# Optimization experiments

Hardware: AMD Instinct MI355X
Metric: run time of the kernel (lower is better)

The kernel has to match this reference:

```python
import jax, jax.numpy as jnp
import numpy as np

NEG = -9e15

def setup_inputs() -> dict:
    key = jax.random.key(0)
    k1, k2, k3, k4 = jax.random.split(key, 4)
    N, Fin, Fout = 8192, 256, 256
    h = jax.random.normal(k1, (N, Fin), dtype=jnp.float32)
    adj = jax.random.randint(k2, (N, N), 0, 2).astype(jnp.float32)
    W = jax.random.normal(k3, (Fin, Fout), dtype=jnp.float32) * (1.414 * np.sqrt(2.0 / (Fin + Fout)))
    a = jax.random.normal(k4, (2 * Fout, 1), dtype=jnp.float32) * (1.414 * np.sqrt(2.0 / (2 * Fout + 1)))
    return {"h": h, "adj": adj, "W": W, "a": a}

def reference(h, adj, W, a):
    Fout = W.shape[1]
    Wh = h @ W                                  # [N, Fout]
    Wh1 = Wh @ a[:Fout, :]                      # [N, 1]
    Wh2 = Wh @ a[Fout:, :]                      # [N, 1]
    e = jax.nn.leaky_relu(Wh1 + Wh2.T, 0.2)     # [N, N]
    mask = (adj > 0).astype(e.dtype)
    e = e * mask + NEG * (1.0 - mask)
    attention = jax.nn.softmax(e, axis=1)       # [N, N]
    h_prime = attention @ Wh                    # [N, Fout]
    return jax.nn.elu(h_prime)
```

## Files before the change

### kernel.cpp

```cpp
#include <hip/hip_runtime.h>
#include <hip/hip_bf16.h>
#include <stdint.h>

typedef __attribute__((ext_vector_type(4))) short short4v;
typedef __attribute__((ext_vector_type(8))) short short8v;
typedef __attribute__((ext_vector_type(4))) float float4v;

#define NN 8192
#define FIN 256
#define FOUT 256

__device__ __forceinline__ short f2bf(float f) {
    unsigned u = __float_as_uint(f);
    unsigned r = u + 0x7fffu + ((u >> 16) & 1u);
    return (short)(r >> 16);
}

__global__ __launch_bounds__(256) void k_wt(const float* __restrict__ W, short* __restrict__ WT) {
    int k = blockIdx.x, n = threadIdx.x;
    WT[n * 256 + k] = f2bf(W[k * 256 + n]);
}

__global__ __launch_bounds__(256) void k_gemm1(const float* __restrict__ h, const short* __restrict__ WT,
                                               float* __restrict__ Wh) {
    __shared__ short sA[64 * 40];
    __shared__ short sB[64 * 40];
    int bm = blockIdx.x;
    int bn = blockIdx.y;
    int t  = threadIdx.x;
    int w = t >> 6, lane = t & 63, quad = lane >> 4, l16 = lane & 15;

    float4v acc[4];
#pragma unroll
    for (int c = 0; c < 4; c++)
#pragma unroll
        for (int j = 0; j < 4; j++) acc[c][j] = 0.f;

    int r  = t >> 2;
    int ko = (t & 3) * 8;

    for (int k0 = 0; k0 < 256; k0 += 32) {
        const float4v* src = (const float4v*)&h[(size_t)(64 * bm + r) * 256 + k0 + ko];
        float4v v0 = src[0], v1 = src[1];
        short8v pk;
        pk[0] = f2bf(v0[0]); pk[1] = f2bf(v0[1]); pk[2] = f2bf(v0[2]); pk[3] = f2bf(v0[3]);
        pk[4] = f2bf(v1[0]); pk[5] = f2bf(v1[1]); pk[6] = f2bf(v1[2]); pk[7] = f2bf(v1[3]);
        *(short8v*)&sA[r * 40 + ko] = pk;
        short8v bv = *(const short8v*)&WT[(size_t)(64 * bn + r) * 256 + k0 + ko];
        *(short8v*)&sB[r * 40 + ko] = bv;
        __syncthreads();

        short8v af = *(const short8v*)&sA[(16 * w + l16) * 40 + quad * 8];
#pragma unroll
        for (int c = 0; c < 4; c++) {
            short8v bf = *(const short8v*)&sB[(16 * c + l16) * 40 + quad * 8];
            acc[c] = __builtin_amdgcn_mfma_f32_16x16x32_bf16(af, bf, acc[c], 0, 0, 0);
        }
        __syncthreads();
    }
#pragma unroll
    for (int c = 0; c < 4; c++)
#pragma unroll
        for (int j = 0; j < 4; j++) {
            int row = 64 * bm + 16 * w + quad * 4 + j;
            int col = 64 * bn + 16 * c + l16;
            Wh[(size_t)row * 256 + col] = acc[c][j];
        }
}

__global__ __launch_bounds__(256) void k_rowstats(const float* __restrict__ Wh, const float* __restrict__ a,
                                                  float* __restrict__ Wh1, float* __restrict__ Wh2,
                                                  unsigned* __restrict__ maxenc) {
    int w = threadIdx.x >> 6, lane = threadIdx.x & 63;
    int row = blockIdx.x * 4 + w;
    float s1 = 0.f, s2 = 0.f;
#pragma unroll
    for (int j = 0; j < 4; j++) {
        int c = lane + 64 * j;
        float v = Wh[(size_t)row * 256 + c];
        s1 += v * a[c];
        s2 += v * a[256 + c];
    }
#pragma unroll
    for (int off = 32; off; off >>= 1) {
        s1 += __shfl_down(s1, off);
        s2 += __shfl_down(s2, off);
    }
    if (lane == 0) {
        Wh1[row] = s1;
        Wh2[row] = s2;
        unsigned u = __float_as_uint(s2);
        unsigned key = (u & 0x80000000u) ? ~u : (u | 0x80000000u);
        atomicMax(maxenc, key);
    }
}

__global__ __launch_bounds__(256) void k_transpose(const float* __restrict__ Wh, short* __restrict__ WhT) {
    __shared__ short sT[64 * 72];
    int bm = blockIdx.x, bn = blockIdx.y;
    int t = threadIdx.x;
#pragma unroll
    for (int i = 0; i < 4; i++) {
        int idx = i * 256 + t;
        int r = idx >> 4, c4 = (idx & 15) * 4;
        float4v v = *(const float4v*)&Wh[(size_t)(64 * bm + r) * 256 + 64 * bn + c4];
#pragma unroll
        for (int j = 0; j < 4; j++) sT[(c4 + j) * 72 + r] = f2bf(v[j]);
    }
    __syncthreads();
    int c = t >> 2, ro = (t & 3) * 16;
#pragma unroll
    for (int hh = 0; hh < 2; hh++) {
        short8v v = *(const short8v*)&sT[c * 72 + ro + 8 * hh];
        *(short8v*)&WhT[(size_t)(64 * bn + c) * 8192 + 64 * bm + ro + 8 * hh] = v;
    }
}

__global__ __launch_bounds__(1024, 4) void k_gat(const float* __restrict__ adj, const short* __restrict__ WhT,
                                                 const float* __restrict__ Wh1, const float* __restrict__ Wh2,
                                                 const unsigned* __restrict__ maxenc,
                                                 float* __restrict__ Cacc, float* __restrict__ Lacc,
                                                 int Ksub) {
    __shared__ short sB[256 * 64];
    __shared__ short sA[64 * 72];
    int bm = blockIdx.x;
    int sidx = blockIdx.y;
    int kb = sidx * Ksub;
    int t = threadIdx.x;
    int lane = t & 63, quad = lane >> 4, l16 = lane & 15;
    int w = t >> 6;
    int rg = w & 3;
    int cg = w >> 2;

    unsigned key = maxenc[0];
    unsigned u = (key & 0x80000000u) ? (key & 0x7fffffffu) : ~key;
    float maxw2 = __uint_as_float(u);

    int r  = t >> 4;
    int kc = (t & 15) * 4;
    float wh1r = Wh1[64 * bm + r];
    float sup = wh1r + maxw2;
    float ci = fmaxf(sup, 0.2f * sup);

    const float* adj_row = &adj[(size_t)(64 * bm + r) * 8192 + kb];
    const float* w2base  = &Wh2[kb];

    int schunk = (t & 7) ^ ((t >> 3) & 7);
    const short* gb0 = &WhT[(size_t)(t >> 3) * 8192 + kb + schunk * 8];
    short* lb0 = &sB[(w * 64 + lane) * 8];

    float4v acc[4];
#pragma unroll
    for (int c = 0; c < 4; c++)
#pragma unroll
        for (int j = 0; j < 4; j++) acc[c][j] = 0.f;
    float lsum = 0.f;

    float4v av = *(const float4v*)&adj_row[kc];
    float4v w2 = *(const float4v*)&w2base[kc];

    for (int k0 = 0; k0 < Ksub; k0 += 64) {
#pragma unroll
        for (int i = 0; i < 2; i++) {
            __builtin_amdgcn_global_load_lds(
                (const __attribute__((address_space(1))) void*)(gb0 + (size_t)i * 128 * 8192 + k0),
                (__attribute__((address_space(3))) void*)(lb0 + i * 1024 * 8),
                16, 0, 0);
        }
        short4v pk;
#pragma unroll
        for (int j = 0; j < 4; j++) {
            float s = wh1r + w2[j];
            float f = fmaxf(s, 0.2f * s);
            float p = __expf(f - ci);
            p = (av[j] > 0.f) ? p : 0.f;
            lsum += p;
            pk[j] = f2bf(p);
        }
        *(short4v*)&sA[r * 72 + kc] = pk;
        if (k0 + 64 < Ksub) {
            av = *(const float4v*)&adj_row[k0 + 64 + kc];
            w2 = *(const float4v*)&w2base[k0 + 64 + kc];
        }
        __syncthreads();

#pragma unroll
        for (int kk = 0; kk < 2; kk++) {
            short8v af = *(const short8v*)&sA[(16 * rg + l16) * 72 + kk * 32 + quad * 8];
#pragma unroll
            for (int c = 0; c < 4; c++) {
                int n = 64 * cg + 16 * c + l16;
                int ch = (kk * 4 + quad) ^ (n & 7);
                short8v bf = *(const short8v*)&sB[n * 64 + ch * 8];
                acc[c] = __builtin_amdgcn_mfma_f32_16x16x32_bf16(af, bf, acc[c], 0, 0, 0);
            }
        }
        __syncthreads();
    }

#pragma unroll
    for (int off = 8; off; off >>= 1) lsum += __shfl_xor(lsum, off, 16);
    if ((lane & 15) == 0) atomicAdd(&Lacc[64 * bm + r], lsum);

#pragma unroll
    for (int c = 0; c < 4; c++)
#pragma unroll
        for (int j = 0; j < 4; j++) {
            int rl = 16 * rg + quad * 4 + j;
            int row = 64 * bm + rl;
            int col = 64 * cg + 16 * c + l16;
            atomicAdd(&Cacc[(size_t)row * 256 + col], acc[c][j]);
        }
}

__global__ __launch_bounds__(256) void k_final(const float* __restrict__ Cacc, const float* __restrict__ Lacc,
                                               float* __restrict__ out) {
    int idx = blockIdx.x * 256 + threadIdx.x;
    int row = idx >> 6;
    int c4 = (idx & 63) * 4;
    float4v v = *(const float4v*)&Cacc[(size_t)row * 256 + c4];
    float inv = 1.0f / fmaxf(Lacc[row], 1e-30f);
    float4v o;
#pragma unroll
    for (int j = 0; j < 4; j++) {
        float x = v[j] * inv;
        o[j] = (x > 0.f) ? x : (__expf(x) - 1.f);
    }
    *(float4v*)&out[(size_t)row * 256 + c4] = o;
}

extern "C" void kernel_launch(void* const* d_in, const int* in_sizes, int n_in,
                              void* d_out, int out_size, void* d_ws, size_t ws_size,
                              hipStream_t stream) {
    const float* h   = (const float*)d_in[0];
    const float* adj = (const float*)d_in[1];
    const float* W   = (const float*)d_in[2];
    const float* a   = (const float*)d_in[3];
    float* out = (float*)d_out;

    const int S = 4;
    const int Ksub = NN / S;

    char* ws = (char*)d_ws;
    float*    Wh     = (float*)(ws);
    float*    Cacc   = (float*)(ws);
    short*    WhT    = (short*)(ws + 8388608);
    char*     tail   = ws + 12582912;
    short*    WT     = (short*)(tail);
    float*    Wh1    = (float*)(tail + 131072);
    float*    Wh2    = (float*)(tail + 163840);
    float*    Lacc   = (float*)(tail + 196608);
    unsigned* maxenc = (unsigned*)(tail + 229376);

    hipMemsetAsync(maxenc, 0, sizeof(unsigned), stream);

    k_wt<<<256, 256, 0, stream>>>(W, WT);
    k_gemm1<<<dim3(128, 4), 256, 0, stream>>>(h, WT, Wh);
    k_rowstats<<<2048, 256, 0, stream>>>(Wh, a, Wh1, Wh2, maxenc);
    k_transpose<<<dim3(128, 4), 256, 0, stream>>>(Wh, WhT);
    hipMemsetAsync(Cacc, 0, (size_t)NN * 256 * sizeof(float), stream);
    hipMemsetAsync(Lacc, 0, (size_t)NN * sizeof(float), stream);
    k_gat<<<dim3(128, S), 1024, 0, stream>>>(adj, WhT, Wh1, Wh2, maxenc, Cacc, Lacc, Ksub);
    k_final<<<2048, 256, 0, stream>>>(Cacc, Lacc, out);
}
```

Measured before the change: 539.9 us.

## Halve k_gat block to 512 threads with 32x64 warp tiles

```diff
diff --git a/kernel.cpp b/kernel.cpp
--- a/kernel.cpp
+++ b/kernel.cpp
@@ -116,11 +116,11 @@
     }
 }
 
-__global__ __launch_bounds__(1024, 4) void k_gat(const float* __restrict__ adj, const short* __restrict__ WhT,
-                                                 const float* __restrict__ Wh1, const float* __restrict__ Wh2,
-                                                 const unsigned* __restrict__ maxenc,
-                                                 float* __restrict__ Cacc, float* __restrict__ Lacc,
-                                                 int Ksub) {
+__global__ __launch_bounds__(512, 4) void k_gat(const float* __restrict__ adj, const short* __restrict__ WhT,
+                                                const float* __restrict__ Wh1, const float* __restrict__ Wh2,
+                                                const unsigned* __restrict__ maxenc,
+                                                float* __restrict__ Cacc, float* __restrict__ Lacc,
+                                                int Ksub) {
     __shared__ short sB[256 * 64];
     __shared__ short sA[64 * 72];
     int bm = blockIdx.x;
@@ -129,15 +129,15 @@
     int t = threadIdx.x;
     int lane = t & 63, quad = lane >> 4, l16 = lane & 15;
     int w = t >> 6;
-    int rg = w & 3;
-    int cg = w >> 2;
+    int mr = (w >> 2) * 32;
+    int cg = w & 3;
 
     unsigned key = maxenc[0];
     unsigned u = (key & 0x80000000u) ? (key & 0x7fffffffu) : ~key;
     float maxw2 = __uint_as_float(u);
 
-    int r  = t >> 4;
-    int kc = (t & 15) * 4;
+    int r  = t >> 3;
+    int kc = (t & 7) * 8;
     float wh1r = Wh1[64 * bm + r];
     float sup = wh1r + maxw2;
     float ci = fmaxf(sup, 0.2f * sup);
@@ -147,70 +147,88 @@
 
     int schunk = (t & 7) ^ ((t >> 3) & 7);
     const short* gb0 = &WhT[(size_t)(t >> 3) * 8192 + kb + schunk * 8];
-    short* lb0 = &sB[(w * 64 + lane) * 8];
-
-    float4v acc[4];
-#pragma unroll
-    for (int c = 0; c < 4; c++)
-#pragma unroll
-        for (int j = 0; j < 4; j++) acc[c][j] = 0.f;
+    short* lb0 = &sB[t * 8];
+
+    float4v acc[2][4];
+#pragma unroll
+    for (int rt = 0; rt < 2; rt++)
+#pragma unroll
+        for (int c = 0; c < 4; c++)
+#pragma unroll
+            for (int j = 0; j < 4; j++) acc[rt][c][j] = 0.f;
     float lsum = 0.f;
 
-    float4v av = *(const float4v*)&adj_row[kc];
-    float4v w2 = *(const float4v*)&w2base[kc];
+    float4v av0 = *(const float4v*)&adj_row[kc];
+    float4v av1 = *(const float4v*)&adj_row[kc + 4];
+    float4v w20 = *(const float4v*)&w2base[kc];
+    float4v w21 = *(const float4v*)&w2base[kc + 4];
 
     for (int k0 = 0; k0 < Ksub; k0 += 64) {
 #pragma unroll
-        for (int i = 0; i < 2; i++) {
+        for (int i = 0; i < 4; i++) {
             __builtin_amdgcn_global_load_lds(
-                (const __attribute__((address_space(1))) void*)(gb0 + (size_t)i * 128 * 8192 + k0),
-                (__attribute__((address_space(3))) void*)(lb0 + i * 1024 * 8),
+                (const __attribute__((address_space(1))) void*)(gb0 + (size_t)i * 64 * 8192 + k0),
+                (__attribute__((address_space(3))) void*)(lb0 + i * 512 * 8),
                 16, 0, 0);
         }
-        short4v pk;
+        short8v pk;
 #pragma unroll
         for (int j = 0; j < 4; j++) {
-            float s = wh1r + w2[j];
+            float s = wh1r + w20[j];
             float f = fmaxf(s, 0.2f * s);
             float p = __expf(f - ci);
-            p = (av[j] > 0.f) ? p : 0.f;
+            p = (av0[j] > 0.f) ? p : 0.f;
             lsum += p;
             pk[j] = f2bf(p);
         }
-        *(short4v*)&sA[r * 72 + kc] = pk;
+#pragma unroll
+        for (int j = 0; j < 4; j++) {
+            float s = wh1r + w21[j];
+            float f = fmaxf(s, 0.2f * s);
+            float p = __expf(f - ci);
+            p = (av1[j] > 0.f) ? p : 0.f;
+            lsum += p;
+            pk[4 + j] = f2bf(p);
+        }
+        *(short8v*)&sA[r * 72 + kc] = pk;
         if (k0 + 64 < Ksub) {
-            av = *(const float4v*)&adj_row[k0 + 64 + kc];
-            w2 = *(const float4v*)&w2base[k0 + 64 + kc];
+            av0 = *(const float4v*)&adj_row[k0 + 64 + kc];
+            av1 = *(const float4v*)&adj_row[k0 + 64 + kc + 4];
+            w20 = *(const float4v*)&w2base[k0 + 64 + kc];
+            w21 = *(const float4v*)&w2base[k0 + 64 + kc + 4];
         }
         __syncthreads();
 
 #pragma unroll
         for (int kk = 0; kk < 2; kk++) {
-            short8v af = *(const short8v*)&sA[(16 * rg + l16) * 72 + kk * 32 + quad * 8];
+            short8v af0 = *(const short8v*)&sA[(mr + l16) * 72 + kk * 32 + quad * 8];
+            short8v af1 = *(const short8v*)&sA[(mr + 16 + l16) * 72 + kk * 32 + quad * 8];
 #pragma unroll
             for (int c = 0; c < 4; c++) {
                 int n = 64 * cg + 16 * c + l16;
                 int ch = (kk * 4 + quad) ^ (n & 7);
                 short8v bf = *(const short8v*)&sB[n * 64 + ch * 8];
-                acc[c] = __builtin_amdgcn_mfma_f32_16x16x32_bf16(af, bf, acc[c], 0, 0, 0);
+                acc[0][c] = __builtin_amdgcn_mfma_f32_16x16x32_bf16(af0, bf, acc[0][c], 0, 0, 0);
+                acc[1][c] = __builtin_amdgcn_mfma_f32_16x16x32_bf16(af1, bf, acc[1][c], 0, 0, 0);
             }
         }
         __syncthreads();
     }
 
 #pragma unroll
-    for (int off = 8; off; off >>= 1) lsum += __shfl_xor(lsum, off, 16);
-    if ((lane & 15) == 0) atomicAdd(&Lacc[64 * bm + r], lsum);
-
-#pragma unroll
-    for (int c = 0; c < 4; c++)
-#pragma unroll
-        for (int j = 0; j < 4; j++) {
-            int rl = 16 * rg + quad * 4 + j;
-            int row = 64 * bm + rl;
-            int col = 64 * cg + 16 * c + l16;
-            atomicAdd(&Cacc[(size_t)row * 256 + col], acc[c][j]);
-        }
+    for (int off = 4; off; off >>= 1) lsum += __shfl_xor(lsum, off, 8);
+    if ((t & 7) == 0) atomicAdd(&Lacc[64 * bm + r], lsum);
+
+#pragma unroll
+    for (int rt = 0; rt < 2; rt++)
+#pragma unroll
+        for (int c = 0; c < 4; c++)
+#pragma unroll
+            for (int j = 0; j < 4; j++) {
+                int row = 64 * bm + mr + rt * 16 + quad * 4 + j;
+                int col = 64 * cg + 16 * c + l16;
+                atomicAdd(&Cacc[(size_t)row * 256 + col], acc[rt][c][j]);
+            }
 }
 
 __global__ __launch_bounds__(256) void k_final(const float* __restrict__ Cacc, const float* __restrict__ Lacc,
@@ -260,6 +278,6 @@
     k_transpose<<<dim3(128, 4), 256, 0, stream>>>(Wh, WhT);
     hipMemsetAsync(Cacc, 0, (size_t)NN * 256 * sizeof(float), stream);
     hipMemsetAsync(Lacc, 0, (size_t)NN * sizeof(float), stream);
-    k_gat<<<dim3(128, S), 1024, 0, stream>>>(adj, WhT, Wh1, Wh2, maxenc, Cacc, Lacc, Ksub);
+    k_gat<<<dim3(128, S), 512, 0, stream>>>(adj, WhT, Wh1, Wh2, maxenc, Cacc, Lacc, Ksub);
     k_final<<<2048, 256, 0, stream>>>(Cacc, Lacc, out);
 }
```

After: 542.8 us. No clear change (+0.5%).

## Register-prefetch WhT tiles and software-pipeline the GAT attention loop

Applied to the files above, without the earlier changes.

```diff
diff --git a/kernel.cpp b/kernel.cpp
--- a/kernel.cpp
+++ b/kernel.cpp
@@ -116,7 +116,7 @@
     }
 }
 
-__global__ __launch_bounds__(1024, 4) void k_gat(const float* __restrict__ adj, const short* __restrict__ WhT,
+__global__ __launch_bounds__(1024, 2) void k_gat(const float* __restrict__ adj, const short* __restrict__ WhT,
                                                  const float* __restrict__ Wh1, const float* __restrict__ Wh2,
                                                  const unsigned* __restrict__ maxenc,
                                                  float* __restrict__ Cacc, float* __restrict__ Lacc,
@@ -145,9 +145,12 @@
     const float* adj_row = &adj[(size_t)(64 * bm + r) * 8192 + kb];
     const float* w2base  = &Wh2[kb];
 
-    int schunk = (t & 7) ^ ((t >> 3) & 7);
-    const short* gb0 = &WhT[(size_t)(t >> 3) * 8192 + kb + schunk * 8];
-    short* lb0 = &sB[(w * 64 + lane) * 8];
+    int nrow = t >> 2;
+    int q = t & 3;
+    const short* gB = &WhT[(size_t)nrow * 8192 + kb + q * 16];
+    int nx = nrow & 7;
+    int sbw0 = nrow * 64 + (((q * 2 + 0) ^ nx)) * 8;
+    int sbw1 = nrow * 64 + (((q * 2 + 1) ^ nx)) * 8;
 
     float4v acc[4];
 #pragma unroll
@@ -156,58 +159,77 @@
         for (int j = 0; j < 4; j++) acc[c][j] = 0.f;
     float lsum = 0.f;
 
-    float4v av = *(const float4v*)&adj_row[kc];
-    float4v w2 = *(const float4v*)&w2base[kc];
-
-    for (int k0 = 0; k0 < Ksub; k0 += 64) {
-#pragma unroll
-        for (int i = 0; i < 2; i++) {
-            __builtin_amdgcn_global_load_lds(
-                (const __attribute__((address_space(1))) void*)(gb0 + (size_t)i * 128 * 8192 + k0),
-                (__attribute__((address_space(3))) void*)(lb0 + i * 1024 * 8),
-                16, 0, 0);
-        }
-        short4v pk;
+    short8v B0, B1;
+    float4v av, avn, w2v;
+
+    av  = *(const float4v*)&adj_row[kc];
+    w2v = *(const float4v*)&w2base[kc];
+    B0 = *(const short8v*)&gB[0];
+    B1 = *(const short8v*)&gB[8];
+    *(short8v*)&sB[sbw0] = B0;
+    *(short8v*)&sB[sbw1] = B1;
+    if (64 < Ksub) {
+        B0 = *(const short8v*)&gB[64];
+        B1 = *(const short8v*)&gB[64 + 8];
+    }
+
+#define STAGE(K0, AV, NAV)                                                                       \
+    {                                                                                            \
+        int k1 = (K0) + 64;                                                                      \
+        if (k1 < Ksub) NAV = *(const float4v*)&adj_row[k1 + kc];                                 \
+        short4v pk;                                                                              \
+        _Pragma("unroll")                                                                        \
+        for (int j = 0; j < 4; j++) {                                                            \
+            float s = wh1r + w2v[j];                                                             \
+            float f = fmaxf(s, 0.2f * s);                                   \
+            float p = __expf(f - ci);                                                            \
+            p = (AV[j] > 0.f) ? p : 0.f;                                                         \
+            lsum += p;                                                                           \
+            pk[j] = f2bf(p);                                                                     \
+        }                                                                                        \
+        *(short4v*)&sA[r * 72 + kc] = pk;                                                        \
+        asm volatile("s_waitcnt lgkmcnt(0)" ::: "memory");                                       \
+        __builtin_amdgcn_s_barrier();                                                            \
+        __builtin_amdgcn_s_setprio(1);                                                           \
+        _Pragma("unroll")                                                                        \
+        for (int kk = 0; kk < 2; kk++) {                                                         \
+            short8v af = *(const short8v*)&sA[(16 * rg + l16) * 72 + kk * 32 + quad * 8];        \
+            _Pragma("unroll")                                                                    \
+            for (int c = 0; c < 4; c++) {                                                        \
+                int n = 64 * cg + 16 * c + l16;                                                  \
+                int ch = (kk * 4 + quad) ^ (n & 7);                                              \
+                short8v bf = *(const short8v*)&sB[n * 64 + ch * 8];                              \
+                acc[c] = __builtin_amdgcn_mfma_f32_16x16x32_bf16(af, bf, acc[c], 0, 0, 0);       \
+            }                                                                                    \
+        }                                                                                        \
+        __builtin_amdgcn_s_setprio(0);                                                           \
+        __builtin_amdgcn_s_barrier();                                                            \
+        if (k1 < Ksub) {                                                                         \
+            *(short8v*)&sB[sbw0] = B0;              \
+            *(short8v*)&sB[sbw1] = B1;                                                           \
+            if (k1 + 64 < Ksub) {                                                                \
+                B0 = *(const short8v*)&gB[k1 + 64];                                              \
+                B1 = *(const short8v*)&gB[k1 + 64 + 8];                                          \
+            }                                                                                    \
+            w2v = *(const float4v*)&w2base[k1 + kc];                \
+        }                                                                                        \
+    }
+
+    for (int k0 = 0; k0 < Ksub; k0 += 128) {
+        STAGE(k0,      av,  avn)
+        STAGE(k0 + 64, avn, av)
+    }
+#undef STAGE
+
+#pragma unroll
+    for (int off = 8; off; off >>= 1) lsum += __shfl_xor(lsum, off, 16);
+    if ((t & 15) == 0) atomicAdd(&Lacc[64 * bm + r], lsum);
+
+#pragma unroll
+    for (int c = 0; c < 4; c++)
 #pragma unroll
         for (int j = 0; j < 4; j++) {
-            float s = wh1r + w2[j];
-            float f = fmaxf(s, 0.2f * s);
-            float p = __expf(f - ci);
-            p = (av[j] > 0.f) ? p : 0.f;
-            lsum += p;
-            pk[j] = f2bf(p);
-        }
-        *(short4v*)&sA[r * 72 + kc] = pk;
-        if (k0 + 64 < Ksub) {
-            av = *(const float4v*)&adj_row[k0 + 64 + kc];
-            w2 = *(const float4v*)&w2base[k0 + 64 + kc];
-        }
-        __syncthreads();
-
-#pragma unroll
-        for (int kk = 0; kk < 2; kk++) {
-            short8v af = *(const short8v*)&sA[(16 * rg + l16) * 72 + kk * 32 + quad * 8];
-#pragma unroll
-            for (int c = 0; c < 4; c++) {
-                int n = 64 * cg + 16 * c + l16;
-                int ch = (kk * 4 + quad) ^ (n & 7);
-                short8v bf = *(const short8v*)&sB[n * 64 + ch * 8];
-                acc[c] = __builtin_amdgcn_mfma_f32_16x16x32_bf16(af, bf, acc[c], 0, 0, 0);
-            }
-        }
-        __syncthreads();
-    }
-
-#pragma unroll
-    for (int off = 8; off; off >>= 1) lsum += __shfl_xor(lsum, off, 16);
-    if ((lane & 15) == 0) atomicAdd(&Lacc[64 * bm + r], lsum);
-
-#pragma unroll
-    for (int c = 0; c < 4; c++)
-#pragma unroll
-        for (int j = 0; j < 4; j++) {
-            int rl = 16 * rg + quad * 4 + j;
-            int row = 64 * bm + rl;
+            int row = 64 * bm + 16 * rg + quad * 4 + j;
             int col = 64 * cg + 16 * c + l16;
             atomicAdd(&Cacc[(size_t)row * 256 + col], acc[c][j]);
         }
```

Result: slower. 573.7 us (+6.3%).
